# Optimization experiments

Measured on AMD Instinct MI355X. Metric: run time of the kernel, lower is better.

The kernel has to match this reference:

```python
import jax, jax.numpy as jnp
import numpy as np

NUM_TREE = 64
TREE_DEPTH = 4
NUM_LEAF = 2 ** (TREE_DEPTH + 1)        # 32
NUM_INTERNALS = NUM_LEAF - 1            # 31
IN_DIM = 512
OUT_DIM = 16
BATCH = 8192


def build_route_masks(tree_depth: int, num_internals: int, num_leaf: int) -> np.ndarray:
    """Static gather indices into the [p, 1-p] concatenated prob vector (length 2*num_internals).
    Returns [tree_depth+1, num_leaf]; product over level axis gives leaf path probabilities.
    Mirrors the increment_mask construction in the torch forward."""
    masks = []
    num_repeat = num_leaf // 2
    num_local_internals = 1
    masks.append(np.repeat(np.array([0, num_internals]), num_repeat))
    for _ in range(1, tree_depth + 1):
        num_repeat //= 2
        num_local_internals *= 2
        m = np.repeat(np.arange(num_local_internals - 1, 2 * num_local_internals - 1), 2)
        m = m + np.tile(np.array([0, num_internals]), num_local_internals)
        m = np.repeat(m, num_repeat)
        masks.append(m)
    return np.stack(masks).astype(np.int32)  # [depth+1, num_leaf]


ROUTE_MASKS = jnp.asarray(build_route_masks(TREE_DEPTH, NUM_INTERNALS, NUM_LEAF))


def setup_inputs() -> dict:
    key = jax.random.key(0)
    k1, k2, k3 = jax.random.split(key, 3)
    x = jax.random.normal(k1, (BATCH, IN_DIM), dtype=jnp.float32)
    # xavier-ish scale so sigmoid gates are not saturated
    W = jax.random.normal(k2, (NUM_TREE * NUM_INTERNALS, IN_DIM), dtype=jnp.float32) / np.sqrt(IN_DIM)
    b = jnp.zeros((NUM_TREE * NUM_INTERNALS,), dtype=jnp.float32)
    leafs = jax.random.normal(k3, (NUM_TREE, NUM_LEAF, OUT_DIM), dtype=jnp.float32)
    return {"x": x, "W": W, "b": b, "leafs": leafs}


def reference(x, W, b, leafs) -> jnp.ndarray:
    B = x.shape[0]
    T, L, O = leafs.shape
    I = L - 1
    tree_net = x @ W.T + b                                  # [B, T*I]
    p = jax.nn.sigmoid(tree_net).reshape(B, T, I)           # split per tree
    flat = jnp.concatenate([p, 1.0 - p], axis=-1)           # [B, T, 2I]
    gathered = flat[:, :, ROUTE_MASKS]                      # [B, T, depth+1, L]
    routes = jnp.prod(gathered, axis=2)                     # [B, T, L] leaf path probs
    leafs_sm = jax.nn.softmax(leafs, axis=-1)
    features = routes.reshape(B, T * L)
    out = features @ leafs_sm.reshape(T * L, O) / T
    return out
```

## Files before the change

kernel.cpp:

```cpp
#include <hip/hip_runtime.h>

#define BATCH 8192
#define IN_DIM 512
#define NT 64
#define NI 31
#define NL 32
#define ODIM 16
#define NPAD (NT*NL)
#define NCB 16

typedef __attribute__((ext_vector_type(8))) short bf16x8;
typedef __attribute__((ext_vector_type(4))) float f32x4;

__device__ __forceinline__ unsigned short f2b(float f) {
  union { float f; unsigned int u; } v; v.f = f;
  unsigned int r = v.u + 0x7fffu + ((v.u >> 16) & 1u);
  return (unsigned short)(r >> 16);
}
__device__ __forceinline__ float b2f(unsigned short h) {
  union { unsigned int u; float f; } v; v.u = ((unsigned int)h) << 16;
  return v.f;
}

__global__ __launch_bounds__(256) void prep_kernel(
    const float* __restrict__ x, const float* __restrict__ W,
    const float* __restrict__ leafs,
    unsigned short* __restrict__ xb, unsigned short* __restrict__ wb,
    float* __restrict__ lsm)
{
  const int NXg = BATCH * (IN_DIM/8);
  const int NWg = NPAD  * (IN_DIM/8);
  const int NS  = NT*NL;
  int gid = blockIdx.x*256 + threadIdx.x;
  if (gid < NXg) {
    int row = gid >> 6, k8 = gid & 63;
    int kt = k8 >> 2, g = k8 & 3;
    int gs = g ^ ((row >> 1) & 3);
    const float* s = x + (size_t)row*IN_DIM + kt*32 + gs*8;
    float4 v0 = ((const float4*)s)[0], v1 = ((const float4*)s)[1];
    ushort4 o0, o1;
    o0.x=f2b(v0.x); o0.y=f2b(v0.y); o0.z=f2b(v0.z); o0.w=f2b(v0.w);
    o1.x=f2b(v1.x); o1.y=f2b(v1.y); o1.z=f2b(v1.z); o1.w=f2b(v1.w);
    ((ushort4*)xb)[gid*2]   = o0;
    ((ushort4*)xb)[gid*2+1] = o1;
  } else if ((gid -= NXg) < NWg) {
    int row = gid >> 6, k8 = gid & 63;
    int t = row >> 5, i = row & 31;
    int kt = k8 >> 2, g = k8 & 3;
    int gs = g ^ ((row >> 1) & 3);
    ushort4 o0, o1;
    if (i == 31) { o0.x=o0.y=o0.z=o0.w=0; o1=o0; }
    else {
      const float* s = W + (size_t)(t*NI+i)*IN_DIM + kt*32 + gs*8;
      float4 v0 = ((const float4*)s)[0], v1 = ((const float4*)s)[1];
      o0.x=f2b(v0.x); o0.y=f2b(v0.y); o0.z=f2b(v0.z); o0.w=f2b(v0.w);
      o1.x=f2b(v1.x); o1.y=f2b(v1.y); o1.z=f2b(v1.z); o1.w=f2b(v1.w);
    }
    ((ushort4*)wb)[gid*2]   = o0;
    ((ushort4*)wb)[gid*2+1] = o1;
  } else if ((gid -= NWg) < NS) {
    const float* src = leafs + (size_t)gid*ODIM;
    float m = src[0];
    #pragma unroll
    for (int o=1;o<ODIM;++o) m = fmaxf(m, src[o]);
    float e[ODIM]; float s = 0.f;
    #pragma unroll
    for (int o=0;o<ODIM;++o) { e[o] = __expf(src[o]-m); s += e[o]; }
    float inv = 1.f/(s*(float)NT);
    #pragma unroll
    for (int o=0;o<ODIM;++o) lsm[(size_t)gid*ODIM+o] = e[o]*inv;
  }
}

__device__ __forceinline__ void async16(const unsigned short* g, unsigned short* l) {
  __builtin_amdgcn_global_load_lds(
      (const __attribute__((address_space(1))) unsigned int*)g,
      (__attribute__((address_space(3))) unsigned int*)l,
      16, 0, 0);
}

#define STG 12288
#define LSM_OFF 66560

__global__ __launch_bounds__(256, 2) void fused_kernel(
    const unsigned short* __restrict__ xb, const unsigned short* __restrict__ wb,
    const float* __restrict__ bias, const float* __restrict__ lsm,
    float* __restrict__ part)
{
  __shared__ __align__(16) unsigned char smem_raw[74752];
  unsigned short* smem = (unsigned short*)smem_raw;
  float* lsmL = (float*)(smem_raw + LSM_OFF);

  const int tid  = threadIdx.x;
  const int lane = tid & 63;
  const int wave = tid >> 6;
  const int wm = wave & 1, wn = wave >> 1;

  const int bid = blockIdx.x;
  const int m_t = (bid & 7)*4 + (bid >> 7);
  const int n_t = (bid >> 3) & 15;
  const int m0 = m_t * 256, n0 = n_t * 128;

  f32x4 acc[8][4];
  #pragma unroll
  for (int i=0;i<8;++i)
    #pragma unroll
    for (int j=0;j<4;++j) { f32x4 z = {0.f,0.f,0.f,0.f}; acc[i][j] = z; }

  const int srow = lane >> 2, scol = (lane & 3) * 8;
  const unsigned short* gaw = xb + (size_t)(m0 + wave*64 + srow)*IN_DIM + scol;
  const unsigned short* gbw = wb + (size_t)(n0 + wave*32 + srow)*IN_DIM + scol;

  const int l15 = lane & 15, quad = lane >> 4;
  const int cs   = (quad ^ ((l15 >> 1) & 3)) << 3;

  #pragma unroll
  for (int c=0;c<4;++c) async16(gaw + c*16*IN_DIM, smem + wave*2048 + c*512);
  #pragma unroll
  for (int c=0;c<2;++c) async16(gbw + c*16*IN_DIM, smem + 8192 + wave*1024 + c*512);

  for (int kt = 0; kt < 16; ++kt) {
    __syncthreads();
    const int cur = (kt & 1) * STG;
    if (kt < 15) {
      const int nxt = ((kt + 1) & 1) * STG;
      const int ko = (kt + 1) * 32;
      #pragma unroll
      for (int c=0;c<4;++c)
        async16(gaw + ko + c*16*IN_DIM, smem + nxt + wave*2048 + c*512);
      #pragma unroll
      for (int c=0;c<2;++c)
        async16(gbw + ko + c*16*IN_DIM, smem + nxt + 8192 + wave*1024 + c*512);
    }
    const unsigned short* As = smem + cur;
    const unsigned short* Bs = smem + cur + 8192;
    bf16x8 af[8], bfr[4];
    #pragma unroll
    for (int mi=0;mi<8;++mi)
      af[mi] = *(const bf16x8*)(As + (wm*128 + mi*16 + l15)*32 + cs);
    #pragma unroll
    for (int ni=0;ni<4;++ni)
      bfr[ni] = *(const bf16x8*)(Bs + (wn*64 + ni*16 + l15)*32 + cs);
    #pragma unroll
    for (int mi=0;mi<8;++mi)
      #pragma unroll
      for (int ni=0;ni<4;++ni)
        acc[mi][ni] = __builtin_amdgcn_mfma_f32_16x16x32_bf16(
            af[mi], bfr[ni], acc[mi][ni], 0, 0, 0);
  }

  const float4* lsm4 = (const float4*)(lsm + (size_t)(n_t*4)*(NL*ODIM));
  float4 lv0 = lsm4[tid], lv1 = lsm4[tid + 256];

  __syncthreads();

  ((float4*)lsmL)[tid]       = lv0;
  ((float4*)lsmL)[tid + 256] = lv1;

  unsigned short* Pt = smem;
  #pragma unroll
  for (int ni=0;ni<4;++ni) {
    int cl = wn*64 + ni*16 + l15;
    int gcol = n0 + cl;
    int tt = gcol >> 5, ii = gcol & 31;
    float bv = (ii < NI) ? bias[tt*NI + ii] : 0.f;
    #pragma unroll
    for (int mi=0;mi<8;++mi) {
      int lrow = wm*128 + mi*16 + quad*4;
      #pragma unroll
      for (int r=0;r<4;++r) {
        float v = acc[mi][ni][r] + bv;
        Pt[(lrow + r)*130 + cl] = f2b(1.f/(1.f + __expf(-v)));
      }
    }
  }
  __syncthreads();

  const int row = tid;
  float oacc[ODIM];
  #pragma unroll
  for (int o=0;o<ODIM;++o) oacc[o] = 0.f;

  #pragma unroll
  for (int tl=0; tl<4; ++tl) {
    const unsigned short* pr = Pt + row*130 + tl*32;
    float v[32];
    float p0 = b2f(pr[0]);
    v[0] = p0; v[1] = 1.f - p0;
    #pragma unroll
    for (int d=1; d<=4; ++d) {
      const int s = 1 << d;
      #pragma unroll
      for (int j=s-1; j>=0; --j) {
        float pj = b2f(pr[(s-1)+j]);
        float base = v[j];
        v[2*j]   = base * pj;
        v[2*j+1] = base * (1.f - pj);
      }
    }
    const float* lp = lsmL + tl*(NL*ODIM);
    #pragma unroll
    for (int l=0;l<NL;++l) {
      float rr = v[l];
      const float4* c4 = (const float4*)(lp + l*ODIM);
      #pragma unroll
      for (int oq=0;oq<4;++oq) {
        float4 c = c4[oq];
        oacc[oq*4+0] += rr*c.x; oacc[oq*4+1] += rr*c.y;
        oacc[oq*4+2] += rr*c.z; oacc[oq*4+3] += rr*c.w;
      }
    }
  }

  float* op = part + ((size_t)n_t*BATCH + (m0 + row))*ODIM;
  #pragma unroll
  for (int oq=0;oq<4;++oq) {
    float4 v; v.x=oacc[oq*4+0]; v.y=oacc[oq*4+1];
    v.z=oacc[oq*4+2]; v.w=oacc[oq*4+3];
    ((float4*)op)[oq] = v;
  }
}

__global__ __launch_bounds__(256) void reduce_kernel(
    const float* __restrict__ part, float* __restrict__ out)
{
  int gid = blockIdx.x*256 + threadIdx.x;
  const float4* p4 = (const float4*)part;
  float4 s = p4[gid];
  #pragma unroll
  for (int cb=1; cb<NCB; ++cb) {
    float4 v = p4[(size_t)cb*(BATCH*ODIM/4) + gid];
    s.x+=v.x; s.y+=v.y; s.z+=v.z; s.w+=v.w;
  }
  ((float4*)out)[gid] = s;
}

extern "C" void kernel_launch(void* const* d_in, const int* in_sizes, int n_in,
                              void* d_out, int out_size, void* d_ws, size_t ws_size,
                              hipStream_t stream) {
  const float* x     = (const float*)d_in[0];
  const float* W     = (const float*)d_in[1];
  const float* b     = (const float*)d_in[2];
  const float* leafs = (const float*)d_in[3];
  float* out = (float*)d_out;

  char* ws = (char*)d_ws;
  unsigned short* xb  = (unsigned short*)ws;
  unsigned short* wb  = (unsigned short*)(ws + 8388608);
  float*          lsm = (float*)(ws + 10485760);
  float*          part= (float*)(ws + 10616832);

  const int total = BATCH*(IN_DIM/8) + NPAD*(IN_DIM/8) + NT*NL;
  prep_kernel<<<dim3((total + 255)/256), dim3(256), 0, stream>>>(
      x, W, leafs, xb, wb, lsm);
  fused_kernel<<<dim3(512), dim3(256), 0, stream>>>(
      xb, wb, b, lsm, part);
  reduce_kernel<<<dim3(BATCH*ODIM/4/256), dim3(256), 0, stream>>>(part, out);
}
```

Baseline: 109.7 us.

## Compute leaf-weighted output with bf16 MFMA instead of scalar FMA loop

```diff
diff --git a/kernel.cpp b/kernel.cpp
--- a/kernel.cpp
+++ b/kernel.cpp
@@ -80,16 +80,13 @@
 }
 
 #define STG 12288
-#define LSM_OFF 66560
 
 __global__ __launch_bounds__(256, 2) void fused_kernel(
     const unsigned short* __restrict__ xb, const unsigned short* __restrict__ wb,
     const float* __restrict__ bias, const float* __restrict__ lsm,
     float* __restrict__ part)
 {
-  __shared__ __align__(16) unsigned char smem_raw[74752];
-  unsigned short* smem = (unsigned short*)smem_raw;
-  float* lsmL = (float*)(smem_raw + LSM_OFF);
+  __shared__ __align__(16) unsigned short smem[34816];
 
   const int tid  = threadIdx.x;
   const int lane = tid & 63;
@@ -149,13 +146,20 @@
             af[mi], bfr[ni], acc[mi][ni], 0, 0, 0);
   }
 
-  const float4* lsm4 = (const float4*)(lsm + (size_t)(n_t*4)*(NL*ODIM));
-  float4 lv0 = lsm4[tid], lv1 = lsm4[tid + 256];
-
-  __syncthreads();
-
-  ((float4*)lsmL)[tid]       = lv0;
-  ((float4*)lsmL)[tid + 256] = lv1;
+  bf16x8 bleaf[4];
+  {
+    const int t0 = n_t * 4;
+    #pragma unroll
+    for (int s=0;s<4;++s) {
+      union { bf16x8 v; unsigned short u[8]; } tmp;
+      #pragma unroll
+      for (int j=0;j<8;++j)
+        tmp.u[j] = f2b(lsm[((size_t)(t0+s)*NL + quad*8 + j)*ODIM + l15]);
+      bleaf[s] = tmp.v;
+    }
+  }
+
+  __syncthreads();
 
   unsigned short* Pt = smem;
   #pragma unroll
@@ -177,47 +181,57 @@
   __syncthreads();
 
   const int row = tid;
-  float oacc[ODIM];
-  #pragma unroll
-  for (int o=0;o<ODIM;++o) oacc[o] = 0.f;
-
+  unsigned int rt[64];
   #pragma unroll
   for (int tl=0; tl<4; ++tl) {
     const unsigned short* pr = Pt + row*130 + tl*32;
+    float q[31];
+    #pragma unroll
+    for (int i=0;i<31;++i) q[i] = b2f(pr[i]);
     float v[32];
-    float p0 = b2f(pr[0]);
-    v[0] = p0; v[1] = 1.f - p0;
+    v[0] = q[0]; v[1] = 1.f - q[0];
     #pragma unroll
     for (int d=1; d<=4; ++d) {
       const int s = 1 << d;
       #pragma unroll
       for (int j=s-1; j>=0; --j) {
-        float pj = b2f(pr[(s-1)+j]);
+        float pj = q[(s-1)+j];
         float base = v[j];
         v[2*j]   = base * pj;
         v[2*j+1] = base * (1.f - pj);
       }
     }
-    const float* lp = lsmL + tl*(NL*ODIM);
-    #pragma unroll
-    for (int l=0;l<NL;++l) {
-      float rr = v[l];
-      const float4* c4 = (const float4*)(lp + l*ODIM);
-      #pragma unroll
-      for (int oq=0;oq<4;++oq) {
-        float4 c = c4[oq];
-        oacc[oq*4+0] += rr*c.x; oacc[oq*4+1] += rr*c.y;
-        oacc[oq*4+2] += rr*c.z; oacc[oq*4+3] += rr*c.w;
-      }
-    }
-  }
-
-  float* op = part + ((size_t)n_t*BATCH + (m0 + row))*ODIM;
-  #pragma unroll
-  for (int oq=0;oq<4;++oq) {
-    float4 v; v.x=oacc[oq*4+0]; v.y=oacc[oq*4+1];
-    v.z=oacc[oq*4+2]; v.w=oacc[oq*4+3];
-    ((float4*)op)[oq] = v;
+    #pragma unroll
+    for (int k=0;k<16;++k)
+      rt[tl*16+k] = (unsigned int)f2b(v[2*k]) | ((unsigned int)f2b(v[2*k+1]) << 16);
+  }
+  __syncthreads();
+
+  unsigned int* Rt32 = (unsigned int*)smem;
+  {
+    uint4* dst = (uint4*)(Rt32 + row*68);
+    #pragma unroll
+    for (int c=0;c<16;++c) {
+      uint4 w; w.x=rt[c*4]; w.y=rt[c*4+1]; w.z=rt[c*4+2]; w.w=rt[c*4+3];
+      dst[c] = w;
+    }
+  }
+  __syncthreads();
+
+  const unsigned short* RtS = smem;
+  #pragma unroll
+  for (int mt=0; mt<4; ++mt) {
+    const int mrow = (wave*4 + mt)*16;
+    f32x4 a2 = {0.f,0.f,0.f,0.f};
+    #pragma unroll
+    for (int s=0;s<4;++s) {
+      bf16x8 af2 = *(const bf16x8*)(RtS + (mrow + l15)*136 + s*32 + quad*8);
+      a2 = __builtin_amdgcn_mfma_f32_16x16x32_bf16(af2, bleaf[s], a2, 0, 0, 0);
+    }
+    float* op = part + ((size_t)n_t*BATCH + (m0 + mrow + quad*4))*ODIM + l15;
+    #pragma unroll
+    for (int r=0;r<4;++r)
+      op[r*ODIM] = a2[r];
   }
 }
 
```

Measured after the change: 104.7 us. -4.6%, faster.
